# Performance work log

Measured on AMD Instinct MI355X. Metric: run time of the kernel, lower is better.

## Reference

```python
import jax, jax.numpy as jnp
import numpy as np

N_NODES = 100000
N_EDGES = 1600000
N_GRAPHS = 4096
BN_EPS = 1e-5


def _gcn_conv(h, src, tgt, deg_inv_sqrt, W, b):
    # GCNConv with self-loops: out_i = sum_{j->i} (d_i d_j)^{-1/2} (XW)_j + d_i^{-1} (XW)_i + b
    h = h @ W                                   # [N, out]
    norm = (deg_inv_sqrt[src] * deg_inv_sqrt[tgt])[:, None]  # [E, 1]
    agg = jax.ops.segment_sum(h[src] * norm, tgt, num_segments=N_NODES)
    agg = agg + h * (deg_inv_sqrt ** 2)[:, None]  # self-loop term
    return agg + b


def _batch_norm(x, gamma, beta):
    # training-mode BatchNorm1d: batch statistics, biased variance
    mean = jnp.mean(x, axis=0)
    var = jnp.mean((x - mean) ** 2, axis=0)
    return (x - mean) * jax.lax.rsqrt(var + BN_EPS) * gamma + beta


def setup_inputs() -> dict:
    key = jax.random.key(0)
    ks = jax.random.split(key, 12)
    x = jax.random.normal(ks[0], (N_NODES, 128), dtype=jnp.float32)
    edge_index = jax.random.randint(ks[1], (2, N_EDGES), 0, N_NODES, dtype=jnp.int32)
    batch = jnp.sort(jax.random.randint(ks[2], (N_NODES,), 0, N_GRAPHS, dtype=jnp.int32))
    def lin(k, fi, fo):
        return jax.random.normal(k, (fi, fo), dtype=jnp.float32) / np.sqrt(fi)
    return {
        "x": x, "edge_index": edge_index, "batch": batch,
        "W1": lin(ks[3], 128, 128), "b1": jnp.zeros((128,), jnp.float32),
        "W2": lin(ks[4], 128, 128), "b2": jnp.zeros((128,), jnp.float32),
        "W3": lin(ks[5], 128, 256), "b3": jnp.zeros((256,), jnp.float32),
        "g1": jnp.ones((128,), jnp.float32), "be1": jnp.zeros((128,), jnp.float32),
        "g2": jnp.ones((128,), jnp.float32), "be2": jnp.zeros((128,), jnp.float32),
    }


def reference(x, edge_index, batch, W1, b1, W2, b2, W3, b3, g1, be1, g2, be2):
    src, tgt = edge_index[0], edge_index[1]
    # degrees including self-loop
    deg = jax.ops.segment_sum(jnp.ones((N_EDGES,), x.dtype), tgt, num_segments=N_NODES) + 1.0
    deg_inv_sqrt = jax.lax.rsqrt(deg)

    h = _gcn_conv(x, src, tgt, deg_inv_sqrt, W1, b1)
    h = jax.nn.relu(_batch_norm(h, g1, be1))          # dropout(p=0.1) as identity (eval)
    h = _gcn_conv(h, src, tgt, deg_inv_sqrt, W2, b2)
    h = jax.nn.relu(_batch_norm(h, g2, be2))
    h = _gcn_conv(h, src, tgt, deg_inv_sqrt, W3, b3)  # [N, 256]

    # global mean pool over batch ids
    sums = jax.ops.segment_sum(h, batch, num_segments=N_GRAPHS)
    counts = jax.ops.segment_sum(jnp.ones((N_NODES,), h.dtype), batch, num_segments=N_GRAPHS)
    return sums / jnp.maximum(counts, 1.0)[:, None]
```

## Files before the change

kernel.cpp:

```cpp
#include <hip/hip_runtime.h>
#include <hip/hip_bf16.h>

#define BN_EPS 1e-5f
#define AGG_BLOCKS 4096
#define BSHIFT 9
#define BUCKN 512
#define NBP 256
#define CB 256

static inline int cdiv(long long a, long long b) { return (int)((a + b - 1) / b); }

typedef __attribute__((ext_vector_type(8))) short short8v;
typedef __attribute__((ext_vector_type(4))) float f32x4;

__device__ __forceinline__ float lo16(int u) {
    return __uint_as_float(((unsigned int)u) << 16);
}
__device__ __forceinline__ float hi16(int u) {
    return __uint_as_float(((unsigned int)u) & 0xffff0000u);
}
__device__ __forceinline__ unsigned short f2bf(float f) {
    unsigned int b = __float_as_uint(f);
    b += 0x7FFFu + ((b >> 16) & 1u);
    return (unsigned short)(b >> 16);
}

__global__ __launch_bounds__(256) void k_bhist(const int* __restrict__ tgt,
                                               int* __restrict__ hcnt, int E, int tile,
                                               int nbuck) {
    __shared__ int lh[NBP];
    const int t = threadIdx.x;
    lh[t] = 0;
    __syncthreads();
    const int base = blockIdx.x * tile;
    const int end = min(base + tile, E);
    for (int i = base + t; i < end; i += 256)
        atomicAdd(&lh[tgt[i] >> BSHIFT], 1);
    __syncthreads();
    if (t < nbuck) hcnt[blockIdx.x * NBP + t] = lh[t];
}

__global__ __launch_bounds__(256) void k_bscan(int* __restrict__ hcnt,
                                               int* __restrict__ btot) {
    const int bucket = blockIdx.x;
    const int t = threadIdx.x;
    __shared__ int sh[256];
    int v = hcnt[t * NBP + bucket];
    sh[t] = v;
    __syncthreads();
    for (int d = 1; d < 256; d <<= 1) {
        int u = (t >= d) ? sh[t - d] : 0;
        __syncthreads();
        sh[t] += u;
        __syncthreads();
    }
    hcnt[t * NBP + bucket] = sh[t] - v;
    if (t == 255) btot[bucket] = sh[255];
}

__global__ __launch_bounds__(256) void k_scan_small(const int* __restrict__ btot,
                                                    int* __restrict__ bbase, int nb) {
    const int t = threadIdx.x;
    __shared__ int sh[256];
    int v = (t < nb) ? btot[t] : 0;
    sh[t] = v;
    __syncthreads();
    for (int d = 1; d < 256; d <<= 1) {
        int u = (t >= d) ? sh[t - d] : 0;
        __syncthreads();
        sh[t] += u;
        __syncthreads();
    }
    if (t < nb) bbase[t] = sh[t] - v;
    if (t == nb) bbase[nb] = sh[255];
    if (t == 255 && nb <= 255) bbase[nb] = sh[255];
}

__global__ __launch_bounds__(256) void k_bscatter2(const int* __restrict__ src,
                                                   const int* __restrict__ tgt,
                                                   const int* __restrict__ hcnt,
                                                   const int* __restrict__ bbase,
                                                   int2* __restrict__ pairs, int E,
                                                   int tile, int nbuck) {
    __shared__ int cur[NBP];
    const int t = threadIdx.x;
    if (t < nbuck) cur[t] = bbase[t] + hcnt[blockIdx.x * NBP + t];
    __syncthreads();
    const int base = blockIdx.x * tile;
    const int end = min(base + tile, E);
    for (int i = base + t; i < end; i += 256) {
        int s = src[i];
        int tg = tgt[i];
        int p = atomicAdd(&cur[tg >> BSHIFT], 1);
        pairs[p] = make_int2(s, tg);
    }
}

__global__ __launch_bounds__(256) void k_bucket_csr(const int2* __restrict__ pairs,
                                                    const int* __restrict__ bbase,
                                                    int* __restrict__ roff,
                                                    float* __restrict__ dis,
                                                    int* __restrict__ esrc,
                                                    int N, int nbuck) {
    __shared__ int cnt[BUCKN];
    __shared__ int cur[BUCKN];
    __shared__ int sh[256];
    const int b = blockIdx.x;
    const int t = threadIdx.x;
    const int nb0 = b * BUCKN;
    cnt[t] = 0;
    cnt[t + 256] = 0;
    __syncthreads();
    const int lo = bbase[b], hi = bbase[b + 1];
    for (int p = lo + t; p < hi; p += 256)
        atomicAdd(&cnt[pairs[p].y - nb0], 1);
    __syncthreads();
    const int c0 = cnt[2 * t], c1 = cnt[2 * t + 1];
    int s = c0 + c1;
    sh[t] = s;
    __syncthreads();
    for (int d = 1; d < 256; d <<= 1) {
        int u = (t >= d) ? sh[t - d] : 0;
        __syncthreads();
        sh[t] += u;
        __syncthreads();
    }
    const int excl = sh[t] - s + lo;
    cur[2 * t] = excl;
    cur[2 * t + 1] = excl + c0;
    const int n0 = nb0 + 2 * t, n1 = n0 + 1;
    if (n0 < N) { roff[n0] = excl; dis[n0] = rsqrtf((float)c0 + 1.0f); }
    if (n1 < N) { roff[n1] = excl + c0; dis[n1] = rsqrtf((float)c1 + 1.0f); }
    if (b == nbuck - 1 && t == 0) roff[N] = hi;
    __syncthreads();
    for (int p = lo + t; p < hi; p += 256) {
        int2 e = pairs[p];
        int q = atomicAdd(&cur[e.y - nb0], 1);
        esrc[q] = e.x;
    }
}

__global__ void k_goff(const int* __restrict__ batch, int* __restrict__ goff,
                       int N, int G) {
    int i = blockIdx.x * blockDim.x + threadIdx.x;
    if (i >= N) return;
    int cur = batch[i];
    int prev = (i == 0) ? -1 : batch[i - 1];
    for (int g = prev + 1; g <= cur; g++) goff[g] = i;
    if (i == N - 1) {
        for (int g = cur + 1; g <= G; g++) goff[g] = N;
    }
}

template <bool BN>
__global__ __launch_bounds__(256) void k_gemm_mfma(const float* __restrict__ X,
                                                   const float* __restrict__ W,
                                                   unsigned short* __restrict__ Y, int N,
                                                   const float* __restrict__ dis,
                                                   const float* __restrict__ sums,
                                                   const float* __restrict__ sumsq,
                                                   const float* __restrict__ g,
                                                   const float* __restrict__ be,
                                                   float inv_n) {
    __shared__ unsigned short As[64][136];
    __shared__ unsigned short Bs[64][136];
    const int t = threadIdx.x;
    const int rbase = blockIdx.x * 64;
    const int cbase = blockIdx.y * 64;

    for (int it = 0; it < 8; it++) {
        int idx = t + it * 256;
        int r = idx >> 5;
        int k4 = (idx & 31) * 4;
        int row = rbase + r;
        float4 v = make_float4(0.f, 0.f, 0.f, 0.f);
        if (row < N) v = *(const float4*)(X + (size_t)row * 128 + k4);
        float o[4] = {v.x, v.y, v.z, v.w};
        if (BN) {
#pragma unroll
            for (int j = 0; j < 4; j++) {
                int c = k4 + j;
                float mean = sums[c] * inv_n;
                float var = sumsq[c] * inv_n - mean * mean;
                float sc = rsqrtf(var + BN_EPS) * g[c];
                o[j] = fmaxf((o[j] - mean) * sc + be[c], 0.0f);
            }
        }
        ushort4 u;
        u.x = f2bf(o[0]); u.y = f2bf(o[1]); u.z = f2bf(o[2]); u.w = f2bf(o[3]);
        *(ushort4*)&As[r][k4] = u;
    }
    for (int it = 0; it < 8; it++) {
        int idx = t + it * 256;
        int k = idx >> 4;
        int c4 = (idx & 15) * 4;
        float4 v = *(const float4*)(W + (size_t)k * 128 + cbase + c4);
        Bs[c4 + 0][k] = f2bf(v.x);
        Bs[c4 + 1][k] = f2bf(v.y);
        Bs[c4 + 2][k] = f2bf(v.z);
        Bs[c4 + 3][k] = f2bf(v.w);
    }
    __syncthreads();

    const int wid = t >> 6;
    const int lane = t & 63;
    const int wr = (wid >> 1) * 32;
    const int wc = (wid & 1) * 32;
    const int lrow = lane & 15;
    const int lkg = lane >> 4;

    f32x4 acc00 = 0, acc01 = 0, acc10 = 0, acc11 = 0;
#pragma unroll
    for (int kk = 0; kk < 4; kk++) {
        const int k0 = kk * 32 + lkg * 8;
        short8v a0 = *(const short8v*)&As[wr + lrow][k0];
        short8v a1 = *(const short8v*)&As[wr + 16 + lrow][k0];
        short8v b0 = *(const short8v*)&Bs[wc + lrow][k0];
        short8v b1 = *(const short8v*)&Bs[wc + 16 + lrow][k0];
        acc00 = __builtin_amdgcn_mfma_f32_16x16x32_bf16(a0, b0, acc00, 0, 0, 0);
        acc01 = __builtin_amdgcn_mfma_f32_16x16x32_bf16(a0, b1, acc01, 0, 0, 0);
        acc10 = __builtin_amdgcn_mfma_f32_16x16x32_bf16(a1, b0, acc10, 0, 0, 0);
        acc11 = __builtin_amdgcn_mfma_f32_16x16x32_bf16(a1, b1, acc11, 0, 0, 0);
    }

#pragma unroll
    for (int rt = 0; rt < 2; rt++) {
        const f32x4 va = rt ? acc10 : acc00;
        const f32x4 vb = rt ? acc11 : acc01;
#pragma unroll
        for (int reg = 0; reg < 4; reg++) {
            int row = rbase + wr + rt * 16 + lkg * 4 + reg;
            if (row < N) {
                float dv = dis[row];
                Y[(size_t)row * 128 + cbase + wc + lrow] = f2bf(va[reg] * dv);
                Y[(size_t)row * 128 + cbase + wc + 16 + lrow] = f2bf(vb[reg] * dv);
            }
        }
    }
}

__global__ __launch_bounds__(256) void k_gemm_final(const float* __restrict__ X,
                                                    const float* __restrict__ W,
                                                    const float* __restrict__ bias,
                                                    const int* __restrict__ goff,
                                                    float* __restrict__ out, int G) {
    __shared__ float xt[128][64];
    __shared__ float wt[128][64];
    const int t = threadIdx.x;
    const int rbase = blockIdx.x * 64;
    const int cbase = blockIdx.y * 64;

    for (int it = 0; it < 8; it++) {
        int idx = t + it * 256;
        int k4 = idx >> 6;
        int r = idx & 63;
        int row = rbase + r;
        float4 v = make_float4(0.f, 0.f, 0.f, 0.f);
        if (row < G) v = *(const float4*)(X + (size_t)row * 128 + k4 * 4);
        xt[k4 * 4 + 0][r] = v.x;
        xt[k4 * 4 + 1][r] = v.y;
        xt[k4 * 4 + 2][r] = v.z;
        xt[k4 * 4 + 3][r] = v.w;
    }
    for (int it = 0; it < 8; it++) {
        int idx = t + it * 256;
        int k = idx >> 4;
        int c4 = (idx & 15) * 4;
        *(float4*)&wt[k][c4] = *(const float4*)(W + (size_t)k * 256 + cbase + c4);
    }
    __syncthreads();

    const int r0 = (t >> 4) * 4;
    const int c0 = (t & 15) * 4;
    float acc[4][4];
#pragma unroll
    for (int i = 0; i < 4; i++)
#pragma unroll
        for (int j = 0; j < 4; j++) acc[i][j] = 0.0f;

#pragma unroll 4
    for (int k = 0; k < 128; k++) {
        float4 a = *(const float4*)&xt[k][r0];
        float4 b = *(const float4*)&wt[k][c0];
        const float av[4] = {a.x, a.y, a.z, a.w};
        const float bv[4] = {b.x, b.y, b.z, b.w};
#pragma unroll
        for (int i = 0; i < 4; i++)
#pragma unroll
            for (int j = 0; j < 4; j++) acc[i][j] += av[i] * bv[j];
    }

#pragma unroll
    for (int i = 0; i < 4; i++) {
        int row = rbase + r0 + i;
        if (row < G) {
            bool empty = (goff[row + 1] == goff[row]);
            float4 o;
            o.x = empty ? 0.f : acc[i][0] + bias[cbase + c0 + 0];
            o.y = empty ? 0.f : acc[i][1] + bias[cbase + c0 + 1];
            o.z = empty ? 0.f : acc[i][2] + bias[cbase + c0 + 2];
            o.w = empty ? 0.f : acc[i][3] + bias[cbase + c0 + 3];
            *(float4*)(out + (size_t)row * 256 + cbase + c0) = o;
        }
    }
}

template <bool STATS>
__global__ __launch_bounds__(256) void k_aggr2(const unsigned short* __restrict__ H,
                                               const int* __restrict__ esrc,
                                               const int* __restrict__ roff,
                                               const float* __restrict__ dis,
                                               const float* __restrict__ bias,
                                               float* __restrict__ out, int N,
                                               float* __restrict__ partial) {
    constexpr int M = 128;
    constexpr int GSZ = 16;
    constexpr int GPB = 16;
    const int nGroups = gridDim.x * GPB;
    const int gid = blockIdx.x * GPB + threadIdx.x / GSZ;
    const int lane = threadIdx.x % GSZ;
    const int c8 = lane * 8;
    const float4 bva = *(const float4*)(bias + c8);
    const float4 bvb = *(const float4*)(bias + c8 + 4);

    float ss[8], sq[8];
    if (STATS) {
#pragma unroll
        for (int k = 0; k < 8; k++) { ss[k] = 0.f; sq[k] = 0.f; }
    }

    for (int n = gid; n < N; n += nGroups) {
        const int rs = roff[n], re = roff[n + 1];
        float acc[8];
#pragma unroll
        for (int j = 0; j < 8; j++) acc[j] = 0.0f;

        int e = rs;
        for (; e + 16 <= re; e += 16) {
            int sid[16];
#pragma unroll
            for (int q = 0; q < 16; q++) sid[q] = esrc[e + q];
            int4 hv[16];
#pragma unroll
            for (int q = 0; q < 16; q++)
                hv[q] = *(const int4*)(H + (size_t)sid[q] * M + c8);
#pragma unroll
            for (int q = 0; q < 16; q++) {
                const int w[4] = {hv[q].x, hv[q].y, hv[q].z, hv[q].w};
#pragma unroll
                for (int k = 0; k < 4; k++) {
                    acc[2 * k + 0] += lo16(w[k]);
                    acc[2 * k + 1] += hi16(w[k]);
                }
            }
        }
        if (e + 8 <= re) {
            int sid[8];
#pragma unroll
            for (int q = 0; q < 8; q++) sid[q] = esrc[e + q];
            int4 hv[8];
#pragma unroll
            for (int q = 0; q < 8; q++)
                hv[q] = *(const int4*)(H + (size_t)sid[q] * M + c8);
#pragma unroll
            for (int q = 0; q < 8; q++) {
                const int w[4] = {hv[q].x, hv[q].y, hv[q].z, hv[q].w};
#pragma unroll
                for (int k = 0; k < 4; k++) {
                    acc[2 * k + 0] += lo16(w[k]);
                    acc[2 * k + 1] += hi16(w[k]);
                }
            }
            e += 8;
        }
        if (e + 4 <= re) {
            int sid[4];
#pragma unroll
            for (int q = 0; q < 4; q++) sid[q] = esrc[e + q];
            int4 hv[4];
#pragma unroll
            for (int q = 0; q < 4; q++)
                hv[q] = *(const int4*)(H + (size_t)sid[q] * M + c8);
#pragma unroll
            for (int q = 0; q < 4; q++) {
                const int w[4] = {hv[q].x, hv[q].y, hv[q].z, hv[q].w};
#pragma unroll
                for (int k = 0; k < 4; k++) {
                    acc[2 * k + 0] += lo16(w[k]);
                    acc[2 * k + 1] += hi16(w[k]);
                }
            }
            e += 4;
        }
        for (; e < re; e++) {
            const int s = esrc[e];
            const int4 h = *(const int4*)(H + (size_t)s * M + c8);
            const int w[4] = {h.x, h.y, h.z, h.w};
#pragma unroll
            for (int k = 0; k < 4; k++) {
                acc[2 * k + 0] += lo16(w[k]);
                acc[2 * k + 1] += hi16(w[k]);
            }
        }
        {
            const int4 h = *(const int4*)(H + (size_t)n * M + c8);
            const int w[4] = {h.x, h.y, h.z, h.w};
#pragma unroll
            for (int k = 0; k < 4; k++) {
                acc[2 * k + 0] += lo16(w[k]);
                acc[2 * k + 1] += hi16(w[k]);
            }
        }
        const float dn = dis[n];
        float ov[8];
#pragma unroll
        for (int k = 0; k < 8; k++) {
            float b = (k < 4) ? (&bva.x)[k] : (&bvb.x)[k - 4];
            ov[k] = acc[k] * dn + b;
            if (STATS) { ss[k] += ov[k]; sq[k] += ov[k] * ov[k]; }
        }
        float4 oa = make_float4(ov[0], ov[1], ov[2], ov[3]);
        float4 ob = make_float4(ov[4], ov[5], ov[6], ov[7]);
        *(float4*)(out + (size_t)n * M + c8) = oa;
        *(float4*)(out + (size_t)n * M + c8 + 4) = ob;
    }

    if (STATS) {
        __shared__ float ls[GPB][256];
        const int g = threadIdx.x / GSZ;
#pragma unroll
        for (int k = 0; k < 8; k++) {
            ls[g][c8 + k] = ss[k];
            ls[g][128 + c8 + k] = sq[k];
        }
        __syncthreads();
        const int f = threadIdx.x;
        float v = 0.f;
#pragma unroll
        for (int gg = 0; gg < GPB; gg++) v += ls[gg][f];
        partial[(size_t)blockIdx.x * 256 + f] = v;
    }
}

__global__ __launch_bounds__(256) void k_redstats(const float* __restrict__ partial,
                                                  float* __restrict__ sums,
                                                  float* __restrict__ sumsq, int nblk) {
    const int f = blockIdx.x;
    const int t = threadIdx.x;
    float v = 0.f;
    for (int b = t; b < nblk; b += 256) v += partial[(size_t)b * 256 + f];
    __shared__ float sh[256];
    sh[t] = v;
    __syncthreads();
    for (int d = 128; d > 0; d >>= 1) {
        if (t < d) sh[t] += sh[t + d];
        __syncthreads();
    }
    if (t == 0) {
        if (f < 128) sums[f] = sh[0];
        else sumsq[f - 128] = sh[0];
    }
}

__global__ void k_bncast(const float* __restrict__ X, const float* __restrict__ sums,
                         const float* __restrict__ sumsq, const float* __restrict__ g,
                         const float* __restrict__ be, const float* __restrict__ dis,
                         unsigned short* __restrict__ Y, long long total4, float inv_n) {
    long long idx = (long long)blockIdx.x * blockDim.x + threadIdx.x;
    if (idx >= total4) return;
    int c4 = ((int)idx & 31) << 2;
    const float dn = dis[(int)(idx >> 5)];
    float4 v = *(const float4*)(X + idx * 4);
    float o[4] = {v.x, v.y, v.z, v.w};
    ushort4 r;
    unsigned short* rp = &r.x;
#pragma unroll
    for (int j = 0; j < 4; j++) {
        int c = c4 + j;
        float mean = sums[c] * inv_n;
        float var = sumsq[c] * inv_n - mean * mean;
        float sc = rsqrtf(var + BN_EPS) * g[c];
        rp[j] = f2bf(fmaxf((o[j] - mean) * sc + be[c], 0.0f) * dn);
    }
    *(ushort4*)(Y + idx * 4) = r;
}

__global__ void k_pool_seg(const float* __restrict__ H, const int* __restrict__ goff,
                           float* __restrict__ out) {
    const int gr = blockIdx.x;
    const int c = threadIdx.x;
    const int s = goff[gr], e = goff[gr + 1];
    float acc = 0.0f;
    for (int i = s; i < e; i++) acc += H[(size_t)i * 128 + c];
    out[(size_t)gr * 128 + c] = acc / fmaxf((float)(e - s), 1.0f);
}

extern "C" void kernel_launch(void* const* d_in, const int* in_sizes, int n_in,
                              void* d_out, int out_size, void* d_ws, size_t ws_size,
                              hipStream_t stream) {
    const float* x     = (const float*)d_in[0];
    const int*   ei    = (const int*)d_in[1];
    const int*   batch = (const int*)d_in[2];
    const float* W1 = (const float*)d_in[3];
    const float* b1 = (const float*)d_in[4];
    const float* W2 = (const float*)d_in[5];
    const float* b2 = (const float*)d_in[6];
    const float* W3 = (const float*)d_in[7];
    const float* b3 = (const float*)d_in[8];
    const float* g1 = (const float*)d_in[9];
    const float* be1 = (const float*)d_in[10];
    const float* g2 = (const float*)d_in[11];
    const float* be2 = (const float*)d_in[12];
    float* out = (float*)d_out;

    const int N = in_sizes[2];
    const int E = in_sizes[1] / 2;
    const int G = out_size / 256;
    const int* src = ei;
    const int* tgt = ei + E;

    char* ws = (char*)d_ws;
    auto take = [&](size_t bytes) {
        char* p = ws;
        ws += (bytes + 255) & ~(size_t)255;
        return p;
    };
    float*          bufB   = (float*)take((size_t)N * 128 * 4);
    unsigned short* bufH   = (unsigned short*)take((size_t)N * 128 * 2);
    float*          P      = (float*)take((size_t)G * 128 * 4);
    float*          dis    = (float*)take((size_t)N * 4);
    float*          sums   = (float*)take(512 * 4);
    float*          sumsq  = sums + 128;
    float*          zbias  = (float*)take(128 * 4);
    float*          partial= (float*)take((size_t)AGG_BLOCKS * 256 * 4);
    int*            roff   = (int*)take((size_t)(N + 1) * 4);
    int*            esrc   = (int*)take((size_t)E * 4);
    int*            goff   = (int*)take((size_t)(G + 1) * 4);
    int*            hcnt   = (int*)take((size_t)CB * NBP * 4);
    int*            btot   = (int*)take(NBP * 4);
    int*            bbase  = (int*)take((NBP + 1) * 4);
    int2*           pairs  = (int2*)bufB;

    const int B = 256;
    const int nbuck = cdiv(N, BUCKN);
    const int tile = cdiv(E, CB);

    hipMemsetAsync(zbias, 0, 128 * 4, stream);

    k_bhist<<<CB, B, 0, stream>>>(tgt, hcnt, E, tile, nbuck);
    k_bscan<<<nbuck, B, 0, stream>>>(hcnt, btot);
    k_scan_small<<<1, B, 0, stream>>>(btot, bbase, nbuck);
    k_bscatter2<<<CB, B, 0, stream>>>(src, tgt, hcnt, bbase, pairs, E, tile, nbuck);
    k_bucket_csr<<<nbuck, B, 0, stream>>>(pairs, bbase, roff, dis, esrc, N, nbuck);
    k_goff<<<cdiv(N, B), B, 0, stream>>>(batch, goff, N, G);

    long long t4_128 = (long long)N * 32;
    const int nbx = cdiv(N, 64);

    k_gemm_mfma<false><<<dim3(nbx, 2), B, 0, stream>>>(x, W1, bufH, N, dis,
                                                       nullptr, nullptr, nullptr, nullptr, 0.f);
    k_aggr2<true><<<AGG_BLOCKS, B, 0, stream>>>(bufH, esrc, roff, dis, b1, bufB, N, partial);
    k_redstats<<<256, B, 0, stream>>>(partial, sums, sumsq, AGG_BLOCKS);

    k_gemm_mfma<true><<<dim3(nbx, 2), B, 0, stream>>>(bufB, W2, bufH, N, dis,
                                                      sums, sumsq, g1, be1, 1.0f / N);
    k_aggr2<true><<<AGG_BLOCKS, B, 0, stream>>>(bufH, esrc, roff, dis, b2, bufB, N, partial);
    k_redstats<<<256, B, 0, stream>>>(partial, sums, sumsq, AGG_BLOCKS);

    k_bncast<<<cdiv(t4_128, B), B, 0, stream>>>(bufB, sums, sumsq, g2, be2, dis, bufH,
                                                t4_128, 1.0f / N);
    k_aggr2<false><<<AGG_BLOCKS, B, 0, stream>>>(bufH, esrc, roff, dis, zbias, bufB, N, nullptr);
    k_pool_seg<<<G, 128, 0, stream>>>(bufB, goff, P);
    k_gemm_final<<<dim3(cdiv(G, 64), 4), B, 0, stream>>>(P, W3, b3, goff, out, G);
}
```

Measured before the change: 387.4 us.

## Fold goff into bucket CSR kernel, drop zbias memset, shrink aggregation unroll and grid

Merges the graph-offset kernel into the bucket CSR launch using extra blocks, and removes the zero-bias memset by passing a null bias pointer that the kernel checks. This cuts two launches from the stream. The aggregation inner loop now unrolls 8 edges instead of 16, which lowers register pressure but leaves fewer gathers in flight. The aggregation grid is halved to 2048 blocks, which also halves the partial-stats buffer.

```diff
diff --git a/kernel.cpp b/kernel.cpp
--- a/kernel.cpp
+++ b/kernel.cpp
@@ -2,7 +2,7 @@
 #include <hip/hip_bf16.h>
 
 #define BN_EPS 1e-5f
-#define AGG_BLOCKS 4096
+#define AGG_BLOCKS 2048
 #define BSHIFT 9
 #define BUCKN 512
 #define NBP 256
@@ -101,12 +101,25 @@
                                                     int* __restrict__ roff,
                                                     float* __restrict__ dis,
                                                     int* __restrict__ esrc,
-                                                    int N, int nbuck) {
+                                                    int N, int nbuck,
+                                                    const int* __restrict__ batch,
+                                                    int* __restrict__ goff, int G) {
+    const int t = threadIdx.x;
+    if ((int)blockIdx.x >= nbuck) {
+        int i = (blockIdx.x - nbuck) * 256 + t;
+        if (i >= N) return;
+        int cur = batch[i];
+        int prev = (i == 0) ? -1 : batch[i - 1];
+        for (int g = prev + 1; g <= cur; g++) goff[g] = i;
+        if (i == N - 1) {
+            for (int g = cur + 1; g <= G; g++) goff[g] = N;
+        }
+        return;
+    }
     __shared__ int cnt[BUCKN];
     __shared__ int cur[BUCKN];
     __shared__ int sh[256];
     const int b = blockIdx.x;
-    const int t = threadIdx.x;
     const int nb0 = b * BUCKN;
     cnt[t] = 0;
     cnt[t + 256] = 0;
@@ -137,18 +150,6 @@
         int2 e = pairs[p];
         int q = atomicAdd(&cur[e.y - nb0], 1);
         esrc[q] = e.x;
-    }
-}
-
-__global__ void k_goff(const int* __restrict__ batch, int* __restrict__ goff,
-                       int N, int G) {
-    int i = blockIdx.x * blockDim.x + threadIdx.x;
-    if (i >= N) return;
-    int cur = batch[i];
-    int prev = (i == 0) ? -1 : batch[i - 1];
-    for (int g = prev + 1; g <= cur; g++) goff[g] = i;
-    if (i == N - 1) {
-        for (int g = cur + 1; g <= G; g++) goff[g] = N;
     }
 }
 
@@ -320,8 +321,12 @@
     const int gid = blockIdx.x * GPB + threadIdx.x / GSZ;
     const int lane = threadIdx.x % GSZ;
     const int c8 = lane * 8;
-    const float4 bva = *(const float4*)(bias + c8);
-    const float4 bvb = *(const float4*)(bias + c8 + 4);
+    float4 bva = make_float4(0.f, 0.f, 0.f, 0.f);
+    float4 bvb = make_float4(0.f, 0.f, 0.f, 0.f);
+    if (bias) {
+        bva = *(const float4*)(bias + c8);
+        bvb = *(const float4*)(bias + c8 + 4);
+    }
 
     float ss[8], sq[8];
     if (STATS) {
@@ -336,16 +341,16 @@
         for (int j = 0; j < 8; j++) acc[j] = 0.0f;
 
         int e = rs;
-        for (; e + 16 <= re; e += 16) {
-            int sid[16];
-#pragma unroll
-            for (int q = 0; q < 16; q++) sid[q] = esrc[e + q];
-            int4 hv[16];
-#pragma unroll
-            for (int q = 0; q < 16; q++)
+        for (; e + 8 <= re; e += 8) {
+            int sid[8];
+#pragma unroll
+            for (int q = 0; q < 8; q++) sid[q] = esrc[e + q];
+            int4 hv[8];
+#pragma unroll
+            for (int q = 0; q < 8; q++)
                 hv[q] = *(const int4*)(H + (size_t)sid[q] * M + c8);
 #pragma unroll
-            for (int q = 0; q < 16; q++) {
+            for (int q = 0; q < 8; q++) {
                 const int w[4] = {hv[q].x, hv[q].y, hv[q].z, hv[q].w};
 #pragma unroll
                 for (int k = 0; k < 4; k++) {
@@ -353,25 +358,6 @@
                     acc[2 * k + 1] += hi16(w[k]);
                 }
             }
-        }
-        if (e + 8 <= re) {
-            int sid[8];
-#pragma unroll
-            for (int q = 0; q < 8; q++) sid[q] = esrc[e + q];
-            int4 hv[8];
-#pragma unroll
-            for (int q = 0; q < 8; q++)
-                hv[q] = *(const int4*)(H + (size_t)sid[q] * M + c8);
-#pragma unroll
-            for (int q = 0; q < 8; q++) {
-                const int w[4] = {hv[q].x, hv[q].y, hv[q].z, hv[q].w};
-#pragma unroll
-                for (int k = 0; k < 4; k++) {
-                    acc[2 * k + 0] += lo16(w[k]);
-                    acc[2 * k + 1] += hi16(w[k]);
-                }
-            }
-            e += 8;
         }
         if (e + 4 <= re) {
             int sid[4];
@@ -531,7 +517,6 @@
     float*          dis    = (float*)take((size_t)N * 4);
     float*          sums   = (float*)take(512 * 4);
     float*          sumsq  = sums + 128;
-    float*          zbias  = (float*)take(128 * 4);
     float*          partial= (float*)take((size_t)AGG_BLOCKS * 256 * 4);
     int*            roff   = (int*)take((size_t)(N + 1) * 4);
     int*            esrc   = (int*)take((size_t)E * 4);
@@ -545,14 +530,12 @@
     const int nbuck = cdiv(N, BUCKN);
     const int tile = cdiv(E, CB);
 
-    hipMemsetAsync(zbias, 0, 128 * 4, stream);
-
     k_bhist<<<CB, B, 0, stream>>>(tgt, hcnt, E, tile, nbuck);
     k_bscan<<<nbuck, B, 0, stream>>>(hcnt, btot);
     k_scan_small<<<1, B, 0, stream>>>(btot, bbase, nbuck);
     k_bscatter2<<<CB, B, 0, stream>>>(src, tgt, hcnt, bbase, pairs, E, tile, nbuck);
-    k_bucket_csr<<<nbuck, B, 0, stream>>>(pairs, bbase, roff, dis, esrc, N, nbuck);
-    k_goff<<<cdiv(N, B), B, 0, stream>>>(batch, goff, N, G);
+    k_bucket_csr<<<nbuck + cdiv(N, B), B, 0, stream>>>(pairs, bbase, roff, dis, esrc,
+                                                       N, nbuck, batch, goff, G);
 
     long long t4_128 = (long long)N * 32;
     const int nbx = cdiv(N, 64);
@@ -569,7 +552,7 @@
 
     k_bncast<<<cdiv(t4_128, B), B, 0, stream>>>(bufB, sums, sumsq, g2, be2, dis, bufH,
                                                 t4_128, 1.0f / N);
-    k_aggr2<false><<<AGG_BLOCKS, B, 0, stream>>>(bufH, esrc, roff, dis, zbias, bufB, N, nullptr);
+    k_aggr2<false><<<AGG_BLOCKS, B, 0, stream>>>(bufH, esrc, roff, dis, nullptr, bufB, N, nullptr);
     k_pool_seg<<<G, 128, 0, stream>>>(bufB, goff, P);
     k_gemm_final<<<dim3(cdiv(G, 64), 4), B, 0, stream>>>(P, W3, b3, goff, out, G);
 }
```

Result: faster. 361.5 us (-6.7%).
